# Optimization experiments

Measured on AMD Instinct MI355X. Metric: run time of the kernel, lower is better.

The kernel has to match this reference:

```python
import jax, jax.numpy as jnp
import numpy as np

N = 50000       # nodes
E = 800000      # edges (before self-loops)
NFEAT = 256
NHID = 16       # per-head hidden dim
HEADS = 8
NCLASS = 16
NEG_SLOPE = 0.2  # PyG GATConv default leaky-relu slope


def setup_inputs() -> dict:
    key = jax.random.key(0)
    ks = jax.random.split(key, 10)
    s = 0.05  # weight scale for numerical sanity
    return {
        "x": jax.random.normal(ks[0], (N, NFEAT), jnp.float32),
        "edge_index": jax.random.randint(ks[1], (2, E), 0, N, dtype=jnp.int32),
        "W1": jax.random.normal(ks[2], (NFEAT, HEADS * NHID), jnp.float32) * s,
        "att_src1": jax.random.normal(ks[3], (HEADS, NHID), jnp.float32) * s,
        "att_dst1": jax.random.normal(ks[4], (HEADS, NHID), jnp.float32) * s,
        "b1": jnp.zeros((HEADS * NHID,), jnp.float32),
        "W2": jax.random.normal(ks[5], (HEADS * NHID, NCLASS), jnp.float32) * s,
        "att_src2": jax.random.normal(ks[6], (1, NCLASS), jnp.float32) * s,
        "att_dst2": jax.random.normal(ks[7], (1, NCLASS), jnp.float32) * s,
        "b2": jnp.zeros((NCLASS,), jnp.float32),
    }


def gat_conv(x, edge_index, W, a_src, a_dst, b, heads, out_c, concat):
    """Faithful PyG GATConv (eval mode: dropout off, add_self_loops=True)."""
    n = x.shape[0]
    loop = jnp.arange(n, dtype=edge_index.dtype)
    src = jnp.concatenate([edge_index[0], loop])  # [E+N]
    dst = jnp.concatenate([edge_index[1], loop])  # [E+N]
    h = (x @ W).reshape(n, heads, out_c)          # [N, H, C]
    # per-node attention logits
    alpha_src = jnp.einsum('nhc,hc->nh', h, a_src)  # [N, H]
    alpha_dst = jnp.einsum('nhc,hc->nh', h, a_dst)  # [N, H]
    e = jax.nn.leaky_relu(alpha_src[src] + alpha_dst[dst], NEG_SLOPE)  # [E+N, H]
    # segment softmax over incoming edges of each dst node (self-loop guarantees nonempty)
    m = jax.lax.stop_gradient(jax.ops.segment_max(e, dst, num_segments=n))
    p = jnp.exp(e - m[dst])
    denom = jax.ops.segment_sum(p, dst, num_segments=n)
    a = p / denom[dst]                              # [E+N, H]
    out = jax.ops.segment_sum(a[:, :, None] * h[src], dst, num_segments=n)  # [N, H, C]
    out = out.reshape(n, heads * out_c) if concat else out.mean(axis=1)
    return out + b


def reference(x, edge_index, W1, att_src1, att_dst1, b1, W2, att_src2, att_dst2, b2):
    h1 = jax.nn.elu(gat_conv(x, edge_index, W1, att_src1, att_dst1, b1, HEADS, NHID, True))
    return gat_conv(h1, edge_index, W2, att_src2, att_dst2, b2, 1, NCLASS, False)
```

## Files before the change

### kernel.cpp

```cpp
#include <hip/hip_runtime.h>
#include <hip/hip_bf16.h>

#define NNODES 50000
#define NEDGES 800000
#define NFEATS 256
#define NHID 16
#define HEADS 8
#define NCLS 16
#define NEG_SLOPE 0.2f
#define TOTE (NEDGES + NNODES)
#define RSTRIDE 64
#define NBUCK 196
#define NPB 256
#define BCAP 4864
#define S1_EPT 16

typedef __attribute__((ext_vector_type(8))) short short8;
typedef __attribute__((ext_vector_type(4))) float floatx4;

static __device__ __forceinline__ short f2bf(float f) {
    __hip_bfloat16 b = __float2bfloat16(f);
    return *reinterpret_cast<short*>(&b);
}

#define AS1 __attribute__((address_space(1)))
#define AS3 __attribute__((address_space(3)))

static __device__ __forceinline__ void ld_lds16(const void* g, void* l) {
#if __has_builtin(__builtin_amdgcn_global_load_lds)
    __builtin_amdgcn_global_load_lds((const AS1 void*)g, (AS3 void*)l, 16, 0, 0);
#endif
}


__global__ __launch_bounds__(256) void k_bin(const int* __restrict__ ei,
                                             int* __restrict__ gcnt, int* __restrict__ barr) {
    __shared__ int lcnt[NBUCK], lbase[NBUCK];
    int tid = threadIdx.x;
    if (tid < NBUCK) lcnt[tid] = 0;
    __syncthreads();
    int e0 = blockIdx.x * (256 * S1_EPT) + tid;
    int s[S1_EPT], d[S1_EPT], rk[S1_EPT];
#pragma unroll
    for (int k = 0; k < S1_EPT; k++) {
        int e = e0 + k * 256;
        bool v = e < TOTE;
        int ss = 0, dd = 0;
        if (v) {
            if (e < NEDGES) { ss = ei[e]; dd = ei[NEDGES + e]; }
            else            { ss = e - NEDGES; dd = ss; }
        }
        s[k] = ss; d[k] = dd;
        rk[k] = v ? atomicAdd(&lcnt[dd >> 8], 1) : -1;
    }
    __syncthreads();
    if (tid < NBUCK) lbase[tid] = lcnt[tid] ? atomicAdd(&gcnt[tid], lcnt[tid]) : 0;
    __syncthreads();
#pragma unroll
    for (int k = 0; k < S1_EPT; k++) {
        if (rk[k] >= 0) {
            int b = d[k] >> 8;
            int pos = lbase[b] + rk[k];
            if (pos < BCAP)
                barr[(size_t)b * BCAP + pos] = ((d[k] & 255) << 16) | s[k];
        }
    }
}


__global__ __launch_bounds__(256) void k_csr(const int* __restrict__ gcnt,
                                             const int* __restrict__ barr,
                                             int* __restrict__ cnt, int* __restrict__ csr) {
    __shared__ int lcnt[NPB];
    __shared__ unsigned short lcsr[NPB * 65];
    int b = blockIdx.x, tid = threadIdx.x;
    lcnt[tid] = 0;
    __syncthreads();
    int n = min(gcnt[b], BCAP);
    int nodeBase = b << 8;
    for (int i = tid; i < n; i += 256) {
        int e = barr[(size_t)b * BCAP + i];
        int ln = e >> 16;
        int r = atomicAdd(&lcnt[ln], 1);
        if (r < RSTRIDE) lcsr[ln * 65 + r] = (unsigned short)(e & 0xFFFF);
    }
    __syncthreads();
    int node = nodeBase + tid;
    if (node < NNODES) cnt[node] = min(lcnt[tid], RSTRIDE);
    for (int i = tid; i < NPB * RSTRIDE; i += 256) {
        int ln = i >> 6;
        int nn = nodeBase + ln;
        if (nn < NNODES && (i & 63) < min(lcnt[ln], RSTRIDE))
            csr[(size_t)nodeBase * RSTRIDE + i] = (int)lcsr[ln * 65 + (i & 63)];
    }
}


__global__ void k_prepw(const float* __restrict__ W, const float* __restrict__ a_s,
                        const float* __restrict__ a_d, short* __restrict__ Wsw) {
    int t = blockIdx.x * 256 + threadIdx.x;
    if (t >= 4608) return;
    short8 b;
    if (t < 4096) {
        int kc = t >> 9, nt = (t >> 6) & 7, lane = t & 63;
        int quad = lane >> 4, lo = lane & 15;
#pragma unroll
        for (int j = 0; j < 8; j++)
            b[j] = f2bf(W[(size_t)(kc * 32 + quad * 8 + j) * 128 + nt * 16 + lo]);
    } else {
        int t2 = t - 4096;
        int kc = t2 >> 6, lane = t2 & 63;
        int quad = lane >> 4, lo = lane & 15;
        int h = lo & 7;
        const float* av = (lo < 8) ? (a_s + h * 16) : (a_d + h * 16);
#pragma unroll
        for (int j = 0; j < 8; j++) {
            int k = kc * 32 + quad * 8 + j;
            float acc = 0.f;
#pragma unroll
            for (int c = 0; c < 16; c++) acc += W[(size_t)k * 128 + h * 16 + c] * av[c];
            b[j] = f2bf(acc);
        }
    }
    *(short8*)(Wsw + (size_t)t * 8) = b;
}


__global__ __launch_bounds__(256) void k_gemm1(const float* __restrict__ x,
                                               const short* __restrict__ Wsw,
                                               __hip_bfloat16* __restrict__ h1,
                                               float* __restrict__ as1, float* __restrict__ ad1) {
    __shared__ short bsw[32768];
    int tid  = threadIdx.x;
    int wave = tid >> 6;
    int lane = tid & 63;
    int quad = lane >> 4;
    int lo   = lane & 15;

#if __has_builtin(__builtin_amdgcn_global_load_lds)
    {
        const char* gsrc = (const char*)Wsw + (size_t)wave * 1024 + (size_t)lane * 16;
        char* ldst = (char*)bsw + wave * 1024;
#pragma unroll
        for (int it = 0; it < 16; it++)
            ld_lds16(gsrc + it * 4096, ldst + it * 4096);
    }
#else
    {
        const uint4* g4 = (const uint4*)Wsw;
        uint4* l4 = (uint4*)bsw;
#pragma unroll
        for (int it = 0; it < 16; it++) l4[it * 256 + tid] = g4[it * 256 + tid];
    }
#endif
    short8 wafr[8];
#pragma unroll
    for (int kc = 0; kc < 8; kc++)
        wafr[kc] = *(const short8*)(Wsw + (size_t)(4096 + kc * 64 + lane) * 8);
    __syncthreads();

    int rowBase = blockIdx.x * 128 + wave * 32;
    const float* xa[2];
#pragma unroll
    for (int mt = 0; mt < 2; mt++) {
        int row = rowBase + mt * 16 + lo;
        row = (row < NNODES) ? row : (NNODES - 1);
        xa[mt] = x + (size_t)row * 256 + quad * 8;
    }

    floatx4 acc[2][8], accA[2];
#pragma unroll
    for (int mt = 0; mt < 2; mt++) {
        accA[mt] = (floatx4){0.f, 0.f, 0.f, 0.f};
#pragma unroll
        for (int nt = 0; nt < 8; nt++) acc[mt][nt] = (floatx4){0.f, 0.f, 0.f, 0.f};
    }

    float4 a0[2], a1[2];
#pragma unroll
    for (int mt = 0; mt < 2; mt++) {
        a0[mt] = *(const float4*)(xa[mt]);
        a1[mt] = *(const float4*)(xa[mt] + 4);
    }

    for (int kc = 0; kc < 8; kc++) {
        float4 n0[2], n1[2];
        if (kc < 7) {
#pragma unroll
            for (int mt = 0; mt < 2; mt++) {
                n0[mt] = *(const float4*)(xa[mt] + (kc + 1) * 32);
                n1[mt] = *(const float4*)(xa[mt] + (kc + 1) * 32 + 4);
            }
        }
        short8 afr[2];
#pragma unroll
        for (int mt = 0; mt < 2; mt++) {
            union { short8 s; __hip_bfloat162 h[4]; } u;
            u.h[0] = __float22bfloat162_rn(make_float2(a0[mt].x, a0[mt].y));
            u.h[1] = __float22bfloat162_rn(make_float2(a0[mt].z, a0[mt].w));
            u.h[2] = __float22bfloat162_rn(make_float2(a1[mt].x, a1[mt].y));
            u.h[3] = __float22bfloat162_rn(make_float2(a1[mt].z, a1[mt].w));
            afr[mt] = u.s;
        }
#pragma unroll
        for (int nt = 0; nt < 8; nt++) {
            short8 bfr = *(const short8*)&bsw[((kc * 8 + nt) * 64 + lane) * 8];
            acc[0][nt] = __builtin_amdgcn_mfma_f32_16x16x32_bf16(afr[0], bfr, acc[0][nt], 0, 0, 0);
            acc[1][nt] = __builtin_amdgcn_mfma_f32_16x16x32_bf16(afr[1], bfr, acc[1][nt], 0, 0, 0);
        }
        accA[0] = __builtin_amdgcn_mfma_f32_16x16x32_bf16(afr[0], wafr[kc], accA[0], 0, 0, 0);
        accA[1] = __builtin_amdgcn_mfma_f32_16x16x32_bf16(afr[1], wafr[kc], accA[1], 0, 0, 0);
#pragma unroll
        for (int mt = 0; mt < 2; mt++) { a0[mt] = n0[mt]; a1[mt] = n1[mt]; }
    }

#pragma unroll
    for (int mt = 0; mt < 2; mt++)
#pragma unroll
        for (int nt = 0; nt < 8; nt++)
#pragma unroll
            for (int reg = 0; reg < 4; reg++) {
                int row = rowBase + mt * 16 + quad * 4 + reg;
                int col = nt * 16 + lo;
                if (row < NNODES)
                    h1[(size_t)row * 128 + col] = __float2bfloat16(acc[mt][nt][reg]);
            }
#pragma unroll
    for (int mt = 0; mt < 2; mt++)
#pragma unroll
        for (int reg = 0; reg < 4; reg++) {
            int row = rowBase + mt * 16 + quad * 4 + reg;
            if (row < NNODES) {
                float v = accA[mt][reg];
                if (lo < 8) as1[(size_t)row * 8 + lo] = v;
                else        ad1[(size_t)row * 8 + (lo - 8)] = v;
            }
        }
}


__global__ __launch_bounds__(256) void k_agg1(const int* __restrict__ cnt, const int* __restrict__ csr,
                                              const __hip_bfloat16* __restrict__ h1,
                                              const float* __restrict__ as1, const float* __restrict__ ad1,
                                              const float* __restrict__ b1, __hip_bfloat16* __restrict__ h1act) {
    int node = blockIdx.x * 4 + (threadIdx.x >> 6);
    int lane = threadIdx.x & 63;
    if (node >= NNODES) return;
    int rs = node * RSTRIDE;
    int deg = min(cnt[node], RSTRIDE);
    int slot = lane >> 4;
    int cl   = lane & 15;
    int head = cl >> 1;
    float adst = ad1[node * 8 + head];
    int rowv = csr[rs + lane];

    float acc[8] = {0.f, 0.f, 0.f, 0.f, 0.f, 0.f, 0.f, 0.f};
    float s = 0.f;
    for (int base = 0; base < deg; base += 16) {
        int src[4]; float p[4];
        union { short8 v; __hip_bfloat162 h[4]; } u[4];
#pragma unroll
        for (int t = 0; t < 4; t++)
            src[t] = __shfl(rowv, base + slot + t * 4);
#pragma unroll
        for (int t = 0; t < 4; t++) {
            p[t] = 0.f;
            u[t].v = (short8){0, 0, 0, 0, 0, 0, 0, 0};
            if (base + slot + t * 4 < deg) {
                u[t].v = *(const short8*)(h1 + (size_t)src[t] * 128 + cl * 8);
                float e = as1[src[t] * 8 + head] + adst;
                e = (e > 0.f) ? e : NEG_SLOPE * e;
                p[t] = __expf(e);
            }
        }
        s += (p[0] + p[1]) + (p[2] + p[3]);
#pragma unroll
        for (int t = 0; t < 4; t++)
#pragma unroll
            for (int q = 0; q < 4; q++) {
                float2 f = __bfloat1622float2(u[t].h[q]);
                acc[q * 2]     = fmaf(p[t], f.x, acc[q * 2]);
                acc[q * 2 + 1] = fmaf(p[t], f.y, acc[q * 2 + 1]);
            }
    }
#pragma unroll
    for (int q = 0; q < 8; q++) {
        acc[q] += __shfl_xor(acc[q], 16);
        acc[q] += __shfl_xor(acc[q], 32);
    }
    s += __shfl_xor(s, 16);
    s += __shfl_xor(s, 32);
    if (slot == 0) {
        float is = 1.f / s;
        union { short8 v; short us[8]; } pk;
#pragma unroll
        for (int q = 0; q < 8; q++) {
            float v = acc[q] * is + b1[cl * 8 + q];
            v = (v > 0.f) ? v : (__expf(v) - 1.f);
            pk.us[q] = f2bf(v);
        }
        *(short8*)(h1act + (size_t)node * 128 + cl * 8) = pk.v;
    }
}


__global__ __launch_bounds__(256) void k_gemm2(const __hip_bfloat16* __restrict__ h1act,
                                               const float* __restrict__ W2,
                                               const float* __restrict__ a_src,
                                               const float* __restrict__ a_dst,
                                               float* __restrict__ h2,
                                               float* __restrict__ as2, float* __restrict__ ad2) {
    __shared__ float w[128 * 16];
    __shared__ float hr[16][129];
    int tid = threadIdx.x;
    int row0 = blockIdx.x * 16;
    for (int i = tid; i < 2048; i += 256) w[i] = W2[i];
    {
        int r = tid >> 4, k8 = (tid & 15) * 8;
        int gr = row0 + r;
        union { short8 v; __hip_bfloat162 h[4]; } u;
        if (gr < NNODES) u.v = *(const short8*)(h1act + (size_t)gr * 128 + k8);
        else             u.v = (short8){0, 0, 0, 0, 0, 0, 0, 0};
#pragma unroll
        for (int q = 0; q < 4; q++) {
            float2 f = __bfloat1622float2(u.h[q]);
            hr[r][k8 + q * 2]     = f.x;
            hr[r][k8 + q * 2 + 1] = f.y;
        }
    }
    __syncthreads();
    int r = tid >> 4, c = tid & 15;
    float acc = 0.f;
#pragma unroll 8
    for (int k = 0; k < 128; k++) acc += hr[r][k] * w[k * 16 + c];
    int gr = row0 + r;
    if (gr < NNODES) h2[(size_t)gr * 16 + c] = acc;
    float sv = acc * a_src[c];
    float dv = acc * a_dst[c];
#pragma unroll
    for (int o = 1; o <= 8; o <<= 1) {
        sv += __shfl_xor(sv, o);
        dv += __shfl_xor(dv, o);
    }
    if (c == 0 && gr < NNODES) { as2[gr] = sv; ad2[gr] = dv; }
}


__global__ __launch_bounds__(256) void k_agg2(const int* __restrict__ cnt, const int* __restrict__ csr,
                                              const float* __restrict__ h2, const float* __restrict__ as2,
                                              const float* __restrict__ ad2, const float* __restrict__ b2,
                                              float* __restrict__ out) {
    int node = blockIdx.x * 4 + (threadIdx.x >> 6);
    int lane = threadIdx.x & 63;
    if (node >= NNODES) return;
    int rs = node * RSTRIDE;
    int deg = min(cnt[node], RSTRIDE);
    int slot = lane >> 2;
    int c4   = lane & 3;
    float adst = ad2[node];
    int rowv = csr[rs + lane];

    float4 acc = make_float4(0.f, 0.f, 0.f, 0.f);
    float s = 0.f;
    for (int base = 0; base < deg; base += 32) {
        int i0 = base + slot, i1 = base + 16 + slot;
        int sa = __shfl(rowv, i0);
        int sb = __shfl(rowv, i1);
        float p0 = 0.f, p1 = 0.f;
        float4 r0 = make_float4(0.f, 0.f, 0.f, 0.f);
        float4 r1 = make_float4(0.f, 0.f, 0.f, 0.f);
        if (i0 < deg) {
            r0 = *(const float4*)(h2 + (size_t)sa * 16 + c4 * 4);
            float e = as2[sa] + adst;
            e = (e > 0.f) ? e : NEG_SLOPE * e;
            p0 = __expf(e);
        }
        if (i1 < deg) {
            r1 = *(const float4*)(h2 + (size_t)sb * 16 + c4 * 4);
            float e = as2[sb] + adst;
            e = (e > 0.f) ? e : NEG_SLOPE * e;
            p1 = __expf(e);
        }
        s += p0 + p1;
        acc.x = fmaf(p0, r0.x, fmaf(p1, r1.x, acc.x));
        acc.y = fmaf(p0, r0.y, fmaf(p1, r1.y, acc.y));
        acc.z = fmaf(p0, r0.z, fmaf(p1, r1.z, acc.z));
        acc.w = fmaf(p0, r0.w, fmaf(p1, r1.w, acc.w));
    }
#pragma unroll
    for (int o = 4; o <= 32; o <<= 1) {
        acc.x += __shfl_xor(acc.x, o);
        acc.y += __shfl_xor(acc.y, o);
        acc.z += __shfl_xor(acc.z, o);
        acc.w += __shfl_xor(acc.w, o);
        s += __shfl_xor(s, o);
    }
    if (slot == 0) {
        float is = 1.f / s;
        float4 o4;
        o4.x = acc.x * is + b2[c4 * 4 + 0];
        o4.y = acc.y * is + b2[c4 * 4 + 1];
        o4.z = acc.z * is + b2[c4 * 4 + 2];
        o4.w = acc.w * is + b2[c4 * 4 + 3];
        *(float4*)(out + (size_t)node * 16 + c4 * 4) = o4;
    }
}


extern "C" void kernel_launch(void* const* d_in, const int* in_sizes, int n_in,
                              void* d_out, int out_size, void* d_ws, size_t ws_size,
                              hipStream_t stream) {
    const float* x    = (const float*)d_in[0];
    const int*   ei   = (const int*)d_in[1];
    const float* W1   = (const float*)d_in[2];
    const float* a_s1 = (const float*)d_in[3];
    const float* a_d1 = (const float*)d_in[4];
    const float* b1   = (const float*)d_in[5];
    const float* W2   = (const float*)d_in[6];
    const float* a_s2 = (const float*)d_in[7];
    const float* a_d2 = (const float*)d_in[8];
    const float* b2   = (const float*)d_in[9];
    float* out = (float*)d_out;

    char* p = (char*)d_ws;
    auto alloc = [&](size_t bytes) -> char* {
        char* q = p;
        p += (bytes + 255) & ~(size_t)255;
        return q;
    };
    int*  gcnt = (int*)alloc(NBUCK * 4);
    int*  barr = (int*)alloc((size_t)NBUCK * BCAP * 4);
    int*  cnt  = (int*)alloc((size_t)NNODES * 4);
    int*  csr  = (int*)alloc((size_t)NNODES * RSTRIDE * 4);
    short* Wsw = (short*)alloc((size_t)36864 * 2);
    __hip_bfloat16* h1 = (__hip_bfloat16*)alloc((size_t)NNODES * 128 * 2);
    float* as1 = (float*)alloc((size_t)NNODES * 8 * 4);
    float* ad1 = (float*)alloc((size_t)NNODES * 8 * 4);
    __hip_bfloat16* h1act = (__hip_bfloat16*)alloc((size_t)NNODES * 128 * 2);
    float* h2  = (float*)as1;
    float* as2 = (float*)barr;
    float* ad2 = (float*)barr + NNODES;

    hipMemsetAsync(gcnt, 0, NBUCK * 4, stream);
    hipLaunchKernelGGL(k_bin,   dim3((TOTE + 4095) / 4096), dim3(256), 0, stream, ei, gcnt, barr);
    hipLaunchKernelGGL(k_csr,   dim3(NBUCK), dim3(256), 0, stream, gcnt, barr, cnt, csr);
    hipLaunchKernelGGL(k_prepw, dim3(18), dim3(256), 0, stream, W1, a_s1, a_d1, Wsw);
    hipLaunchKernelGGL(k_gemm1, dim3((NNODES + 127) / 128), dim3(256), 0, stream, x, Wsw, h1, as1, ad1);
    hipLaunchKernelGGL(k_agg1,  dim3((NNODES + 3) / 4), dim3(256), 0, stream, cnt, csr, h1, as1, ad1, b1, h1act);
    hipLaunchKernelGGL(k_gemm2, dim3((NNODES + 15) / 16), dim3(256), 0, stream, h1act, W2, a_s2, a_d2, h2, as2, ad2);
    hipLaunchKernelGGL(k_agg2,  dim3((NNODES + 3) / 4), dim3(256), 0, stream, cnt, csr, h2, as2, ad2, b2, out);
}
```

Before: 225.8 us.

## Process four destination nodes per wavefront in both aggregation kernels

Both aggregation kernels now map four nodes to each 64-lane wavefront, one per 16-lane group, instead of one node per wavefront split into edge slots. Each group walks its own node's edge list, so the cross-slot shuffle reductions go away in agg1 and shrink in agg2, and the grid becomes a quarter the size. The loop runs to the maximum degree among the four nodes, so groups whose node has fewer edges idle, and the bounds check is dropped because NNODES divides evenly by 16.

```diff
diff --git a/kernel.cpp b/kernel.cpp
--- a/kernel.cpp
+++ b/kernel.cpp
@@ -243,64 +243,65 @@
                                               const __hip_bfloat16* __restrict__ h1,
                                               const float* __restrict__ as1, const float* __restrict__ ad1,
                                               const float* __restrict__ b1, __hip_bfloat16* __restrict__ h1act) {
-    int node = blockIdx.x * 4 + (threadIdx.x >> 6);
+    int wid  = blockIdx.x * 4 + (threadIdx.x >> 6);
     int lane = threadIdx.x & 63;
-    if (node >= NNODES) return;
-    int rs = node * RSTRIDE;
-    int deg = min(cnt[node], RSTRIDE);
-    int slot = lane >> 4;
+    int grp  = lane >> 4;
     int cl   = lane & 15;
+    int node = wid * 4 + grp;
+    int deg  = min(cnt[node], RSTRIDE);
     int head = cl >> 1;
     float adst = ad1[node * 8 + head];
-    int rowv = csr[rs + lane];
+    int rs = node * RSTRIDE;
+    int rowv[4];
+#pragma unroll
+    for (int r = 0; r < 4; r++) rowv[r] = csr[rs + cl + 16 * r];
+    int md = deg;
+    md = max(md, __shfl_xor(md, 16));
+    md = max(md, __shfl_xor(md, 32));
 
     float acc[8] = {0.f, 0.f, 0.f, 0.f, 0.f, 0.f, 0.f, 0.f};
     float s = 0.f;
-    for (int base = 0; base < deg; base += 16) {
-        int src[4]; float p[4];
-        union { short8 v; __hip_bfloat162 h[4]; } u[4];
-#pragma unroll
-        for (int t = 0; t < 4; t++)
-            src[t] = __shfl(rowv, base + slot + t * 4);
-#pragma unroll
-        for (int t = 0; t < 4; t++) {
-            p[t] = 0.f;
-            u[t].v = (short8){0, 0, 0, 0, 0, 0, 0, 0};
-            if (base + slot + t * 4 < deg) {
-                u[t].v = *(const short8*)(h1 + (size_t)src[t] * 128 + cl * 8);
-                float e = as1[src[t] * 8 + head] + adst;
-                e = (e > 0.f) ? e : NEG_SLOPE * e;
-                p[t] = __expf(e);
-            }
-        }
-        s += (p[0] + p[1]) + (p[2] + p[3]);
-#pragma unroll
-        for (int t = 0; t < 4; t++)
-#pragma unroll
-            for (int q = 0; q < 4; q++) {
-                float2 f = __bfloat1622float2(u[t].h[q]);
-                acc[q * 2]     = fmaf(p[t], f.x, acc[q * 2]);
-                acc[q * 2 + 1] = fmaf(p[t], f.y, acc[q * 2 + 1]);
-            }
-    }
+#pragma unroll
+    for (int r = 0; r < 4; r++) {
+        int rbase = r << 4;
+        if (rbase >= md) break;
+        int lim = min(16, md - rbase);
+        for (int i2 = 0; i2 < lim; i2 += 4) {
+            float p[4];
+            union { short8 v; __hip_bfloat162 h[4]; } u[4];
+#pragma unroll
+            for (int t = 0; t < 4; t++) {
+                int idx = rbase + i2 + t;
+                int src = __shfl(rowv[r], (lane & 48) | (idx & 15));
+                p[t] = 0.f;
+                u[t].v = (short8){0, 0, 0, 0, 0, 0, 0, 0};
+                if (idx < deg) {
+                    u[t].v = *(const short8*)(h1 + (size_t)src * 128 + cl * 8);
+                    float e = as1[src * 8 + head] + adst;
+                    e = (e > 0.f) ? e : NEG_SLOPE * e;
+                    p[t] = __expf(e);
+                }
+            }
+            s += (p[0] + p[1]) + (p[2] + p[3]);
+#pragma unroll
+            for (int t = 0; t < 4; t++)
+#pragma unroll
+                for (int q = 0; q < 4; q++) {
+                    float2 f = __bfloat1622float2(u[t].h[q]);
+                    acc[q * 2]     = fmaf(p[t], f.x, acc[q * 2]);
+                    acc[q * 2 + 1] = fmaf(p[t], f.y, acc[q * 2 + 1]);
+                }
+        }
+    }
+    float is = 1.f / s;
+    union { short8 v; short us[8]; } pk;
 #pragma unroll
     for (int q = 0; q < 8; q++) {
-        acc[q] += __shfl_xor(acc[q], 16);
-        acc[q] += __shfl_xor(acc[q], 32);
-    }
-    s += __shfl_xor(s, 16);
-    s += __shfl_xor(s, 32);
-    if (slot == 0) {
-        float is = 1.f / s;
-        union { short8 v; short us[8]; } pk;
-#pragma unroll
-        for (int q = 0; q < 8; q++) {
-            float v = acc[q] * is + b1[cl * 8 + q];
-            v = (v > 0.f) ? v : (__expf(v) - 1.f);
-            pk.us[q] = f2bf(v);
-        }
-        *(short8*)(h1act + (size_t)node * 128 + cl * 8) = pk.v;
-    }
+        float v = acc[q] * is + b1[cl * 8 + q];
+        v = (v > 0.f) ? v : (__expf(v) - 1.f);
+        pk.us[q] = f2bf(v);
+    }
+    *(short8*)(h1act + (size_t)node * 128 + cl * 8) = pk.v;
 }
 
 
@@ -350,45 +351,59 @@
                                               const float* __restrict__ h2, const float* __restrict__ as2,
                                               const float* __restrict__ ad2, const float* __restrict__ b2,
                                               float* __restrict__ out) {
-    int node = blockIdx.x * 4 + (threadIdx.x >> 6);
+    int wid  = blockIdx.x * 4 + (threadIdx.x >> 6);
     int lane = threadIdx.x & 63;
-    if (node >= NNODES) return;
+    int grp  = lane >> 4;
+    int sub  = lane & 15;
+    int slot = sub >> 2;
+    int c4   = sub & 3;
+    int node = wid * 4 + grp;
+    int deg  = min(cnt[node], RSTRIDE);
+    float adst = ad2[node];
     int rs = node * RSTRIDE;
-    int deg = min(cnt[node], RSTRIDE);
-    int slot = lane >> 2;
-    int c4   = lane & 3;
-    float adst = ad2[node];
-    int rowv = csr[rs + lane];
+    int rowv[4];
+#pragma unroll
+    for (int r = 0; r < 4; r++) rowv[r] = csr[rs + sub + 16 * r];
+    int md = deg;
+    md = max(md, __shfl_xor(md, 16));
+    md = max(md, __shfl_xor(md, 32));
 
     float4 acc = make_float4(0.f, 0.f, 0.f, 0.f);
     float s = 0.f;
-    for (int base = 0; base < deg; base += 32) {
-        int i0 = base + slot, i1 = base + 16 + slot;
-        int sa = __shfl(rowv, i0);
-        int sb = __shfl(rowv, i1);
-        float p0 = 0.f, p1 = 0.f;
-        float4 r0 = make_float4(0.f, 0.f, 0.f, 0.f);
-        float4 r1 = make_float4(0.f, 0.f, 0.f, 0.f);
-        if (i0 < deg) {
-            r0 = *(const float4*)(h2 + (size_t)sa * 16 + c4 * 4);
-            float e = as2[sa] + adst;
-            e = (e > 0.f) ? e : NEG_SLOPE * e;
-            p0 = __expf(e);
-        }
-        if (i1 < deg) {
-            r1 = *(const float4*)(h2 + (size_t)sb * 16 + c4 * 4);
-            float e = as2[sb] + adst;
-            e = (e > 0.f) ? e : NEG_SLOPE * e;
-            p1 = __expf(e);
-        }
-        s += p0 + p1;
-        acc.x = fmaf(p0, r0.x, fmaf(p1, r1.x, acc.x));
-        acc.y = fmaf(p0, r0.y, fmaf(p1, r1.y, acc.y));
-        acc.z = fmaf(p0, r0.z, fmaf(p1, r1.z, acc.z));
-        acc.w = fmaf(p0, r0.w, fmaf(p1, r1.w, acc.w));
-    }
-#pragma unroll
-    for (int o = 4; o <= 32; o <<= 1) {
+#pragma unroll
+    for (int r = 0; r < 4; r++) {
+        int rbase = r << 4;
+        if (rbase >= md) break;
+        int lim = min(16, md - rbase);
+        for (int i2 = 0; i2 < lim; i2 += 8) {
+            int ia = rbase + i2 + slot;
+            int ib = ia + 4;
+            int sa = __shfl(rowv[r], (lane & 48) | ((i2 + slot) & 15));
+            int sb = __shfl(rowv[r], (lane & 48) | ((i2 + 4 + slot) & 15));
+            float p0 = 0.f, p1 = 0.f;
+            float4 r0 = make_float4(0.f, 0.f, 0.f, 0.f);
+            float4 r1 = make_float4(0.f, 0.f, 0.f, 0.f);
+            if (ia < deg) {
+                r0 = *(const float4*)(h2 + (size_t)sa * 16 + c4 * 4);
+                float e = as2[sa] + adst;
+                e = (e > 0.f) ? e : NEG_SLOPE * e;
+                p0 = __expf(e);
+            }
+            if (ib < deg) {
+                r1 = *(const float4*)(h2 + (size_t)sb * 16 + c4 * 4);
+                float e = as2[sb] + adst;
+                e = (e > 0.f) ? e : NEG_SLOPE * e;
+                p1 = __expf(e);
+            }
+            s += p0 + p1;
+            acc.x = fmaf(p0, r0.x, fmaf(p1, r1.x, acc.x));
+            acc.y = fmaf(p0, r0.y, fmaf(p1, r1.y, acc.y));
+            acc.z = fmaf(p0, r0.z, fmaf(p1, r1.z, acc.z));
+            acc.w = fmaf(p0, r0.w, fmaf(p1, r1.w, acc.w));
+        }
+    }
+#pragma unroll
+    for (int o = 4; o <= 8; o <<= 1) {
         acc.x += __shfl_xor(acc.x, o);
         acc.y += __shfl_xor(acc.y, o);
         acc.z += __shfl_xor(acc.z, o);
@@ -446,7 +461,7 @@
     hipLaunchKernelGGL(k_csr,   dim3(NBUCK), dim3(256), 0, stream, gcnt, barr, cnt, csr);
     hipLaunchKernelGGL(k_prepw, dim3(18), dim3(256), 0, stream, W1, a_s1, a_d1, Wsw);
     hipLaunchKernelGGL(k_gemm1, dim3((NNODES + 127) / 128), dim3(256), 0, stream, x, Wsw, h1, as1, ad1);
-    hipLaunchKernelGGL(k_agg1,  dim3((NNODES + 3) / 4), dim3(256), 0, stream, cnt, csr, h1, as1, ad1, b1, h1act);
+    hipLaunchKernelGGL(k_agg1,  dim3(NNODES / 16), dim3(256), 0, stream, cnt, csr, h1, as1, ad1, b1, h1act);
     hipLaunchKernelGGL(k_gemm2, dim3((NNODES + 15) / 16), dim3(256), 0, stream, h1act, W2, a_s2, a_d2, h2, as2, ad2);
-    hipLaunchKernelGGL(k_agg2,  dim3((NNODES + 3) / 4), dim3(256), 0, stream, cnt, csr, h2, as2, ad2, b2, out);
-}
+    hipLaunchKernelGGL(k_agg2,  dim3(NNODES / 16), dim3(256), 0, stream, cnt, csr, h2, as2, ad2, b2, out);
+}
```

Measured after the change: 220.8 us. 2.2% less time.
